# Kernel optimization log

Measured on AMD Instinct MI355X. Metric: run time of the kernel, lower is better.

Reference implementation:

```python
import jax, jax.numpy as jnp
import numpy as np
from jax import lax

B, H, W, C = 8, 128, 128, 256


def setup_inputs() -> dict:
    key = jax.random.key(0)
    k1, k2 = jax.random.split(key)
    x = jax.random.normal(k1, (B, H, W, C), dtype=jnp.float32)
    # small-magnitude kernel so predicted offsets stay moderate (like trained init)
    kernel = jax.random.normal(k2, (3, 3, C, 2 * C), dtype=jnp.float32) * 0.01
    bias = jnp.zeros((2 * C,), dtype=jnp.float32)
    return {"x": x, "kernel": kernel, "bias": bias}


def _deform_sample(x, kernel, bias):
    b, h, w, c = x.shape
    # offset prediction conv: (b,h,w,c) -> (b,h,w,2c), SAME padding, stride 1
    offsets = lax.conv_general_dilated(
        x, kernel, window_strides=(1, 1), padding="SAME",
        dimension_numbers=("NHWC", "HWIO", "NHWC")) + bias
    # faithful reshape scaffolding from the original keras layer
    # (b,h,w,2c) -> (b,2c,h,w) -> (b*c, h, w, 2)
    offs = jnp.transpose(offsets, (0, 3, 1, 2)).reshape(b * c, h, w, 2)
    # (b,h,w,c) -> (b*c, h, w)
    xb = jnp.transpose(x, (0, 3, 1, 2)).reshape(b * c, h, w)

    n = h * w
    offs = offs.reshape(b * c, n, 2)
    grid = jnp.stack(jnp.meshgrid(jnp.arange(h), jnp.arange(w), indexing="ij"), axis=-1)
    grid = grid.reshape(n, 2).astype(x.dtype)  # (n,2) absolute (i,j)
    coords = offs + grid  # (b*c, n, 2)

    # original clips coord0 by w-1 and coord1 by h-1 (h==w assumed)
    c0 = jnp.clip(coords[..., 0], 0.0, jnp.float32(w - 1))
    c1 = jnp.clip(coords[..., 1], 0.0, jnp.float32(h - 1))
    coords = jnp.stack([c0, c1], axis=-1)

    lt = jnp.floor(coords).astype(jnp.int32)  # (b*c, n, 2)
    rb = jnp.ceil(coords).astype(jnp.int32)

    bidx = jnp.arange(b * c)[:, None]  # (b*c, 1) broadcast over n
    vals_lt = xb[bidx, lt[..., 0], lt[..., 1]]
    vals_rb = xb[bidx, rb[..., 0], rb[..., 1]]
    vals_lb = xb[bidx, lt[..., 0], rb[..., 1]]
    vals_rt = xb[bidx, rb[..., 0], lt[..., 1]]

    frac = coords - lt.astype(coords.dtype)  # (b*c, n, 2)
    vals_t = vals_lt + (vals_rt - vals_lt) * frac[..., 0]
    vals_b = vals_lb + (vals_rb - vals_lb) * frac[..., 0]
    mapped = vals_t + (vals_b - vals_t) * frac[..., 1]  # (b*c, n)

    # (b*c, h*w) -> (b, c, h, w) -> (b, h, w, c)
    return jnp.transpose(mapped.reshape(b, c, h, w), (0, 2, 3, 1))


def reference(x, kernel, bias):
    return _deform_sample(x, kernel, bias)
```

## Files before the change

kernel.cpp:

```cpp
#include <hip/hip_runtime.h>
#include <hip/hip_bf16.h>

#define BATCH 8
#define HH 128
#define WW 128
#define CC 256
#define OCC 512

typedef __bf16 bf16x8 __attribute__((ext_vector_type(8)));
typedef float f32x4 __attribute__((ext_vector_type(4)));

__global__ void prep_weights(const float* __restrict__ k, __bf16* __restrict__ wt) {
    int idx = blockIdx.x * 256 + threadIdx.x;
    int oc   = idx & 511;
    int rest = idx >> 9;
    int ic   = rest & 255;
    int tap  = rest >> 8;
    wt[(tap * OCC + oc) * CC + ic] = (__bf16)k[idx];
}

__global__ __launch_bounds__(256, 2)
void conv_offset_sample(const float* __restrict__ x, const __bf16* __restrict__ wt,
                        const float* __restrict__ bias, float* __restrict__ out) {
    const int bi  = blockIdx.x;
    const int ncb = bi & 3;
    const int cr  = (bi >> 2) & 127;
    const int b   = bi >> 9;
    const int oc0 = ncb * 128;

    const int tid  = threadIdx.x;
    const int lane = tid & 63;
    const int wid  = tid >> 6;
    const int wm   = wid >> 1;
    const int wn   = wid & 1;
    const int l15  = lane & 15;
    const int lg   = lane >> 4;

    const float* xb = x + (size_t)b * (HH * WW * CC);

    f32x4 acc[4][4] = {};

#pragma unroll 1
    for (int tap = 0; tap < 9; ++tap) {
        const int dy = tap / 3 - 1;
        const int dx = tap - (tap / 3) * 3 - 1;
        const int row = cr + dy;
        const bool rowok = (unsigned)row < (unsigned)HH;
        const float* xrow = xb + row * (WW * CC);
        const __bf16* wtap = wt + (size_t)tap * (OCC * CC);

        for (int icc = 0; icc < CC; icc += 32) {
            const int ic = icc + lg * 8;

            bf16x8 afrag[4];
#pragma unroll
            for (int mi = 0; mi < 4; ++mi) {
                const int col = wm * 64 + mi * 16 + l15 + dx;
                f32x4 v0 = {0.f, 0.f, 0.f, 0.f};
                f32x4 v1 = {0.f, 0.f, 0.f, 0.f};
                if (rowok && (unsigned)col < (unsigned)WW) {
                    const f32x4* p = (const f32x4*)(xrow + col * CC + ic);
                    v0 = p[0];
                    v1 = p[1];
                }
                bf16x8 a;
                a[0] = (__bf16)v0[0]; a[1] = (__bf16)v0[1];
                a[2] = (__bf16)v0[2]; a[3] = (__bf16)v0[3];
                a[4] = (__bf16)v1[0]; a[5] = (__bf16)v1[1];
                a[6] = (__bf16)v1[2]; a[7] = (__bf16)v1[3];
                afrag[mi] = a;
            }

            bf16x8 bfrag[4];
#pragma unroll
            for (int ni = 0; ni < 4; ++ni) {
                const int oc = oc0 + wn * 64 + ni * 16 + l15;
                bfrag[ni] = *(const bf16x8*)(wtap + oc * CC + ic);
            }

#pragma unroll
            for (int mi = 0; mi < 4; ++mi)
#pragma unroll
                for (int ni = 0; ni < 4; ++ni)
                    acc[mi][ni] = __builtin_amdgcn_mfma_f32_16x16x32_bf16(
                        afrag[mi], bfrag[ni], acc[mi][ni], 0, 0, 0);
        }
    }

    const int ibase = cr >> 1;
    const int jbase = (cr & 1) * 64;

#pragma unroll
    for (int ni = 0; ni < 4; ++ni) {
        const int oc = oc0 + wn * 64 + ni * 16 + l15;
        const float bv = bias[oc];
        const int p  = oc >> 1;
        const int i2 = ibase + ((oc & 1) << 6);
        const float* xp = x + (size_t)b * (HH * WW * CC) + p;
        float* op = out + (((size_t)b * HH + i2) * WW) * CC + p;

#pragma unroll
        for (int mi = 0; mi < 4; ++mi) {
#pragma unroll
            for (int s = 0; s < 2; ++s) {
                const int u  = wm * 32 + mi * 8 + lg * 2 + s;
                const int j2 = jbase + u;

                float c0 = acc[mi][ni][2 * s]     + bv + (float)i2;
                float c1 = acc[mi][ni][2 * s + 1] + bv + (float)j2;
                c0 = fminf(fmaxf(c0, 0.f), 127.f);
                c1 = fminf(fmaxf(c1, 0.f), 127.f);

                const int lt0 = (int)floorf(c0);
                const int rb0 = (int)ceilf(c0);
                const int lt1 = (int)floorf(c1);
                const int rb1 = (int)ceilf(c1);
                const float f0 = c0 - (float)lt0;
                const float f1 = c1 - (float)lt1;

                const float vlt = xp[(lt0 * WW + lt1) * CC];
                const float vrb = xp[(rb0 * WW + rb1) * CC];
                const float vlb = xp[(lt0 * WW + rb1) * CC];
                const float vrt = xp[(rb0 * WW + lt1) * CC];

                const float vt = vlt + (vrt - vlt) * f0;
                const float vb = vlb + (vrb - vlb) * f0;
                op[(size_t)j2 * CC] = vt + (vb - vt) * f1;
            }
        }
    }
}

extern "C" void kernel_launch(void* const* d_in, const int* in_sizes, int n_in,
                              void* d_out, int out_size, void* d_ws, size_t ws_size,
                              hipStream_t stream) {
    const float* x    = (const float*)d_in[0];
    const float* kern = (const float*)d_in[1];
    const float* bias = (const float*)d_in[2];
    float* out = (float*)d_out;
    __bf16* wt = (__bf16*)d_ws;

    prep_weights<<<4608, 256, 0, stream>>>(kern, wt);
    conv_offset_sample<<<4096, 256, 0, stream>>>(x, wt, bias, out);
}
```

Measured before the change: 1.811 ms.

## Add planar transposed copy of x for gather sampling and reorder weight columns

Adds a transpose kernel that writes x in channel-planar layout (b,c,h*w) into workspace, so the bilinear gathers within a channel plane touch nearby addresses instead of addresses strided by 256 floats. Weight prep now permutes output channels so each block's N-tile groups channels by offset parity, which changes the channel-to-lane mapping in the epilogue. The transpose costs an extra full read and write of x (about 128MB each way) and needs a large workspace; if the workspace is too small the code falls back to the old interleaved layout. Launch bounds drop the min-blocks hint.

New measurement: 1.949 ms. 1.08x slower.

```diff
diff --git a/kernel.cpp b/kernel.cpp
--- a/kernel.cpp
+++ b/kernel.cpp
@@ -11,22 +11,49 @@
 typedef float f32x4 __attribute__((ext_vector_type(4)));
 
 __global__ void prep_weights(const float* __restrict__ k, __bf16* __restrict__ wt) {
-    int idx = blockIdx.x * 256 + threadIdx.x;
-    int oc   = idx & 511;
-    int rest = idx >> 9;
-    int ic   = rest & 255;
-    int tap  = rest >> 8;
-    wt[(tap * OCC + oc) * CC + ic] = (__bf16)k[idx];
+    const int n   = blockIdx.x & 511;
+    const int tap = blockIdx.x >> 9;
+    const int ic  = threadIdx.x;
+    const int oc  = ((n & 255) << 1) | (n >> 8);
+    wt[((size_t)(tap * OCC + n)) * CC + ic] = (__bf16)k[((size_t)(tap * CC + ic)) * OCC + oc];
 }
 
-__global__ __launch_bounds__(256, 2)
-void conv_offset_sample(const float* __restrict__ x, const __bf16* __restrict__ wt,
+__global__ __launch_bounds__(256)
+void transpose_x(const float* __restrict__ x, float* __restrict__ xt) {
+    __shared__ float tile[64][65];
+    const int pt = blockIdx.x & 3;
+    const int mt = (blockIdx.x >> 2) & 255;
+    const int b  = blockIdx.x >> 10;
+    const int m0 = mt * 64;
+    const int p0 = pt * 64;
+    const int tl = threadIdx.x & 63;
+    const int tr = threadIdx.x >> 6;
+
+    const float* xb = x + (size_t)b * (HH * WW * CC);
+#pragma unroll
+    for (int rr = 0; rr < 16; ++rr) {
+        const int m = rr * 4 + tr;
+        tile[m][tl] = xb[(size_t)(m0 + m) * CC + p0 + tl];
+    }
+    __syncthreads();
+    float* xtb = xt + (size_t)b * (CC * HH * WW);
+#pragma unroll
+    for (int rr = 0; rr < 16; ++rr) {
+        const int p = rr * 4 + tr;
+        xtb[(size_t)(p0 + p) * (HH * WW) + m0 + tl] = tile[tl][p];
+    }
+}
+
+template <bool PLANAR>
+__global__ __launch_bounds__(256)
+void conv_offset_sample(const float* __restrict__ x, const float* __restrict__ xt,
+                        const __bf16* __restrict__ wt,
                         const float* __restrict__ bias, float* __restrict__ out) {
     const int bi  = blockIdx.x;
     const int ncb = bi & 3;
     const int cr  = (bi >> 2) & 127;
     const int b   = bi >> 9;
-    const int oc0 = ncb * 128;
+    const int n0  = ncb * 128;
 
     const int tid  = threadIdx.x;
     const int lane = tid & 63;
@@ -74,8 +101,8 @@
             bf16x8 bfrag[4];
 #pragma unroll
             for (int ni = 0; ni < 4; ++ni) {
-                const int oc = oc0 + wn * 64 + ni * 16 + l15;
-                bfrag[ni] = *(const bf16x8*)(wtap + oc * CC + ic);
+                const int n = n0 + wn * 64 + ni * 16 + l15;
+                bfrag[ni] = *(const bf16x8*)(wtap + (size_t)n * CC + ic);
             }
 
 #pragma unroll
@@ -92,11 +119,18 @@
 
 #pragma unroll
     for (int ni = 0; ni < 4; ++ni) {
-        const int oc = oc0 + wn * 64 + ni * 16 + l15;
-        const float bv = bias[oc];
-        const int p  = oc >> 1;
-        const int i2 = ibase + ((oc & 1) << 6);
-        const float* xp = x + (size_t)b * (HH * WW * CC) + p;
+        const int n   = n0 + wn * 64 + ni * 16 + l15;
+        const int p   = n & 255;
+        const int par = n >> 8;
+        const int i2  = ibase + (par << 6);
+        const float bv = bias[2 * p + par];
+
+        const float* plane;
+        if (PLANAR) {
+            plane = xt + (size_t)(b * CC + p) * (HH * WW);
+        } else {
+            plane = x + (size_t)b * (HH * WW * CC) + p;
+        }
         float* op = out + (((size_t)b * HH + i2) * WW) * CC + p;
 
 #pragma unroll
@@ -118,10 +152,18 @@
                 const float f0 = c0 - (float)lt0;
                 const float f1 = c1 - (float)lt1;
 
-                const float vlt = xp[(lt0 * WW + lt1) * CC];
-                const float vrb = xp[(rb0 * WW + rb1) * CC];
-                const float vlb = xp[(lt0 * WW + rb1) * CC];
-                const float vrt = xp[(rb0 * WW + lt1) * CC];
+                float vlt, vrb, vlb, vrt;
+                if (PLANAR) {
+                    vlt = plane[(lt0 << 7) + lt1];
+                    vrb = plane[(rb0 << 7) + rb1];
+                    vlb = plane[(lt0 << 7) + rb1];
+                    vrt = plane[(rb0 << 7) + lt1];
+                } else {
+                    vlt = plane[((lt0 << 7) + lt1) << 8];
+                    vrb = plane[((rb0 << 7) + rb1) << 8];
+                    vlb = plane[((lt0 << 7) + rb1) << 8];
+                    vrt = plane[((rb0 << 7) + lt1) << 8];
+                }
 
                 const float vt = vlt + (vrt - vlt) * f0;
                 const float vb = vlb + (vrb - vlb) * f0;
@@ -138,8 +180,18 @@
     const float* kern = (const float*)d_in[1];
     const float* bias = (const float*)d_in[2];
     float* out = (float*)d_out;
+
     __bf16* wt = (__bf16*)d_ws;
+    const size_t XT_OFF = 4u * 1024u * 1024u;
+    const size_t XT_BYTES = (size_t)BATCH * CC * HH * WW * 4;
+    float* xt = (float*)((char*)d_ws + XT_OFF);
+    const bool planar = (ws_size >= XT_OFF + XT_BYTES);
 
     prep_weights<<<4608, 256, 0, stream>>>(kern, wt);
-    conv_offset_sample<<<4096, 256, 0, stream>>>(x, wt, bias, out);
+    if (planar) {
+        transpose_x<<<8192, 256, 0, stream>>>(x, xt);
+        conv_offset_sample<true><<<4096, 256, 0, stream>>>(x, xt, wt, bias, out);
+    } else {
+        conv_offset_sample<false><<<4096, 256, 0, stream>>>(x, xt, wt, bias, out);
+    }
 }
```

## Stage bf16 input rows in LDS and gather from a channel-planar bf16 copy

Applied to the files above, without the earlier changes.

Adds a prep pass that converts x to bf16 twice: once in NHWC layout and once transposed into per-channel planes. The conv kernel now stages whole bf16 input rows into double-buffered LDS with async global-to-LDS loads and an XOR swizzle. Each staged row is reused across the three horizontal taps, and the wave tiling changes to 2x8. The bilinear gather now reads 2-byte values from contiguous per-channel planes, replacing strided fp32 loads, and the block order is remapped. This trades extra prep passes and workspace traffic for less global load traffic, no per-tap fp32-to-bf16 conversion, and better gather locality. Gathered values are now bf16 rather than fp32, which lowers output precision.

Measured after the change: 1.488 ms. 1.22x faster.

```diff
diff --git a/kernel.cpp b/kernel.cpp
--- a/kernel.cpp
+++ b/kernel.cpp
@@ -8,105 +8,159 @@
 #define OCC 512
 
 typedef __bf16 bf16x8 __attribute__((ext_vector_type(8)));
+typedef unsigned int u32x4 __attribute__((ext_vector_type(4)));
 typedef float f32x4 __attribute__((ext_vector_type(4)));
 
+#define WT_OFF   0
+#define ZROW_OFF 2359296
+#define XTB_OFF  2424832
+#define XBF_OFF  69533696
+
 __global__ void prep_weights(const float* __restrict__ k, __bf16* __restrict__ wt) {
-    int idx = blockIdx.x * 256 + threadIdx.x;
-    int oc   = idx & 511;
-    int rest = idx >> 9;
-    int ic   = rest & 255;
-    int tap  = rest >> 8;
-    wt[(tap * OCC + oc) * CC + ic] = (__bf16)k[idx];
+    const int n   = blockIdx.x & 511;
+    const int tap = blockIdx.x >> 9;
+    const int ic  = threadIdx.x;
+    const int oc  = ((n & 255) << 1) | (n >> 8);
+    wt[((size_t)(tap * OCC + n)) * CC + ic] = (__bf16)k[((size_t)(tap * CC + ic)) * OCC + oc];
+}
+
+__global__ void zero_fill(float* __restrict__ z) {
+    z[blockIdx.x * 256 + threadIdx.x] = 0.0f;
+}
+
+__global__ __launch_bounds__(256)
+void prep_x(const float* __restrict__ x, __bf16* __restrict__ xbf, __bf16* __restrict__ xtb) {
+    __shared__ float tile[64][65];
+    const int pt = blockIdx.x & 3;
+    const int mt = (blockIdx.x >> 2) & 255;
+    const int b  = blockIdx.x >> 10;
+    const int m0 = mt * 64, p0 = pt * 64;
+    const int tl = threadIdx.x & 63, tr = threadIdx.x >> 6;
+
+    const float* xb = x + (size_t)b * (HH * WW * CC);
+    __bf16* xbfb = xbf + (size_t)b * (HH * WW * CC);
+#pragma unroll
+    for (int rr = 0; rr < 16; ++rr) {
+        const int m = rr * 4 + tr;
+        const float v = xb[(size_t)(m0 + m) * CC + p0 + tl];
+        tile[m][tl] = v;
+        xbfb[(size_t)(m0 + m) * CC + p0 + tl] = (__bf16)v;
+    }
+    __syncthreads();
+    __bf16* xtbb = xtb + (size_t)b * (CC * HH * WW);
+#pragma unroll
+    for (int rr = 0; rr < 16; ++rr) {
+        const int p = rr * 4 + tr;
+        xtbb[(size_t)(p0 + p) * (HH * WW) + m0 + tl] = (__bf16)tile[tl][p];
+    }
+}
+
+__device__ __forceinline__ void gload16(const void* g, void* l) {
+    __builtin_amdgcn_global_load_lds(
+        (const __attribute__((address_space(1))) void*)g,
+        (__attribute__((address_space(3))) void*)l, 16, 0, 0);
+}
+
+__device__ __forceinline__ void stage_chunk(const __bf16* __restrict__ srcrow, int h,
+                                            __bf16* ldsbuf, int wid, int lane) {
+    const int sub = lane >> 4;
+    const int icb = (lane & 15) * 16;
+#pragma unroll
+    for (int t = 0; t < 8; ++t) {
+        const int col = (wid * 8 + t) * 4 + sub;
+        const int srcoff = col * 512 + h * 256 + (icb ^ ((col & 7) << 4));
+        gload16((const char*)srcrow + srcoff, (char*)ldsbuf + (wid * 8 + t) * 1024);
+    }
 }
 
 __global__ __launch_bounds__(256, 2)
-void conv_offset_sample(const float* __restrict__ x, const __bf16* __restrict__ wt,
+void conv_offset_sample(const __bf16* __restrict__ xbf, const __bf16* __restrict__ xtb,
+                        const __bf16* __restrict__ zrow, const __bf16* __restrict__ wt,
                         const float* __restrict__ bias, float* __restrict__ out) {
-    const int bi  = blockIdx.x;
-    const int ncb = bi & 3;
-    const int cr  = (bi >> 2) & 127;
-    const int b   = bi >> 9;
-    const int oc0 = ncb * 128;
+    __shared__ __bf16 lds_a[2][16384];
+
+    const int orig = blockIdx.x;
+    const int bi = (orig & 7) * 512 + (orig >> 3);
+    const int nc = bi & 3;
+    const int cr = (bi >> 2) & 127;
+    const int b  = bi >> 9;
 
     const int tid  = threadIdx.x;
     const int lane = tid & 63;
     const int wid  = tid >> 6;
-    const int wm   = wid >> 1;
-    const int wn   = wid & 1;
     const int l15  = lane & 15;
     const int lg   = lane >> 4;
 
-    const float* xb = x + (size_t)b * (HH * WW * CC);
-
-    f32x4 acc[4][4] = {};
-
+    f32x4 acc[2][8] = {};
+
+    {
+        const int rg = cr - 1;
+        const __bf16* srcrow = ((unsigned)rg < 128u) ? xbf + ((size_t)(b * 128 + rg) << 15) : zrow;
+        stage_chunk(srcrow, 0, lds_a[0], wid, lane);
+    }
+    __syncthreads();
+
+    int cur = 0;
 #pragma unroll 1
-    for (int tap = 0; tap < 9; ++tap) {
-        const int dy = tap / 3 - 1;
-        const int dx = tap - (tap / 3) * 3 - 1;
-        const int row = cr + dy;
-        const bool rowok = (unsigned)row < (unsigned)HH;
-        const float* xrow = xb + row * (WW * CC);
-        const __bf16* wtap = wt + (size_t)tap * (OCC * CC);
-
-        for (int icc = 0; icc < CC; icc += 32) {
-            const int ic = icc + lg * 8;
-
-            bf16x8 afrag[4];
-#pragma unroll
-            for (int mi = 0; mi < 4; ++mi) {
-                const int col = wm * 64 + mi * 16 + l15 + dx;
-                f32x4 v0 = {0.f, 0.f, 0.f, 0.f};
-                f32x4 v1 = {0.f, 0.f, 0.f, 0.f};
-                if (rowok && (unsigned)col < (unsigned)WW) {
-                    const f32x4* p = (const f32x4*)(xrow + col * CC + ic);
-                    v0 = p[0];
-                    v1 = p[1];
+    for (int idx = 0; idx < 6; ++idx) {
+        if (idx < 5) {
+            const int n2 = idx + 1;
+            const int rg = cr + (n2 >> 1) - 1;
+            const __bf16* srcrow = ((unsigned)rg < 128u) ? xbf + ((size_t)(b * 128 + rg) << 15) : zrow;
+            stage_chunk(srcrow, n2 & 1, lds_a[cur ^ 1], wid, lane);
+        }
+        const int r = idx >> 1;
+        const int h = idx & 1;
+        const __bf16* Ab = lds_a[cur];
+        const int colb = wid * 32;
+
+#pragma unroll
+        for (int dx = 0; dx < 3; ++dx) {
+            const __bf16* wtap = wt + ((size_t)((r * 3 + dx) * OCC + nc * 128)) * CC + h * 128;
+#pragma unroll
+            for (int kk = 0; kk < 4; ++kk) {
+                bf16x8 a[2];
+#pragma unroll
+                for (int mi = 0; mi < 2; ++mi) {
+                    const int ca = colb + mi * 16 + l15 + dx - 1;
+                    const unsigned msk = ((unsigned)ca < 128u) ? 0xFFFFFFFFu : 0u;
+                    const int ad = (((ca & 127) << 8) + ((kk * 32 + lg * 8) << 1)) ^ ((ca & 7) << 4);
+                    u32x4 uv = *(const u32x4*)((const char*)Ab + ad);
+                    uv &= msk;
+                    a[mi] = __builtin_bit_cast(bf16x8, uv);
                 }
-                bf16x8 a;
-                a[0] = (__bf16)v0[0]; a[1] = (__bf16)v0[1];
-                a[2] = (__bf16)v0[2]; a[3] = (__bf16)v0[3];
-                a[4] = (__bf16)v1[0]; a[5] = (__bf16)v1[1];
-                a[6] = (__bf16)v1[2]; a[7] = (__bf16)v1[3];
-                afrag[mi] = a;
+#pragma unroll
+                for (int ni = 0; ni < 8; ++ni) {
+                    const bf16x8 bv = *(const bf16x8*)(wtap + (ni * 16 + l15) * CC + kk * 32 + lg * 8);
+                    acc[0][ni] = __builtin_amdgcn_mfma_f32_16x16x32_bf16(a[0], bv, acc[0][ni], 0, 0, 0);
+                    acc[1][ni] = __builtin_amdgcn_mfma_f32_16x16x32_bf16(a[1], bv, acc[1][ni], 0, 0, 0);
+                }
             }
-
-            bf16x8 bfrag[4];
-#pragma unroll
-            for (int ni = 0; ni < 4; ++ni) {
-                const int oc = oc0 + wn * 64 + ni * 16 + l15;
-                bfrag[ni] = *(const bf16x8*)(wtap + oc * CC + ic);
-            }
-
-#pragma unroll
-            for (int mi = 0; mi < 4; ++mi)
-#pragma unroll
-                for (int ni = 0; ni < 4; ++ni)
-                    acc[mi][ni] = __builtin_amdgcn_mfma_f32_16x16x32_bf16(
-                        afrag[mi], bfrag[ni], acc[mi][ni], 0, 0, 0);
         }
-    }
-
-    const int ibase = cr >> 1;
-    const int jbase = (cr & 1) * 64;
-
-#pragma unroll
-    for (int ni = 0; ni < 4; ++ni) {
-        const int oc = oc0 + wn * 64 + ni * 16 + l15;
-        const float bv = bias[oc];
-        const int p  = oc >> 1;
-        const int i2 = ibase + ((oc & 1) << 6);
-        const float* xp = x + (size_t)b * (HH * WW * CC) + p;
-        float* op = out + (((size_t)b * HH + i2) * WW) * CC + p;
-
-#pragma unroll
-        for (int mi = 0; mi < 4; ++mi) {
+        __syncthreads();
+        cur ^= 1;
+    }
+
+    const int jbase = (cr & 1) << 6;
+    const int par = nc >> 1;
+    const int i2  = (cr >> 1) + (par << 6);
+    const float fi2 = (float)i2;
+
+#pragma unroll
+    for (int ni = 0; ni < 8; ++ni) {
+        const int p = ((nc & 1) << 7) + ni * 16 + l15;
+        const float bv = bias[2 * p + par];
+        const __bf16* plane = xtb + ((size_t)(b * 256 + p) << 14);
+        float* op = out + (((size_t)(b * 128 + i2)) << 7) * 256 + p;
+
+#pragma unroll
+        for (int mi = 0; mi < 2; ++mi) {
 #pragma unroll
             for (int s = 0; s < 2; ++s) {
-                const int u  = wm * 32 + mi * 8 + lg * 2 + s;
+                const int u  = wid * 16 + mi * 8 + lg * 2 + s;
                 const int j2 = jbase + u;
 
-                float c0 = acc[mi][ni][2 * s]     + bv + (float)i2;
+                float c0 = acc[mi][ni][2 * s]     + bv + fi2;
                 float c1 = acc[mi][ni][2 * s + 1] + bv + (float)j2;
                 c0 = fminf(fmaxf(c0, 0.f), 127.f);
                 c1 = fminf(fmaxf(c1, 0.f), 127.f);
@@ -118,14 +172,14 @@
                 const float f0 = c0 - (float)lt0;
                 const float f1 = c1 - (float)lt1;
 
-                const float vlt = xp[(lt0 * WW + lt1) * CC];
-                const float vrb = xp[(rb0 * WW + rb1) * CC];
-                const float vlb = xp[(lt0 * WW + rb1) * CC];
-                const float vrt = xp[(rb0 * WW + lt1) * CC];
+                const float vlt = (float)plane[(lt0 << 7) + lt1];
+                const float vrb = (float)plane[(rb0 << 7) + rb1];
+                const float vlb = (float)plane[(lt0 << 7) + rb1];
+                const float vrt = (float)plane[(rb0 << 7) + lt1];
 
                 const float vt = vlt + (vrt - vlt) * f0;
                 const float vb = vlb + (vrb - vlb) * f0;
-                op[(size_t)j2 * CC] = vt + (vb - vt) * f1;
+                op[(size_t)j2 * 256] = vt + (vb - vt) * f1;
             }
         }
     }
@@ -138,8 +192,14 @@
     const float* kern = (const float*)d_in[1];
     const float* bias = (const float*)d_in[2];
     float* out = (float*)d_out;
-    __bf16* wt = (__bf16*)d_ws;
+
+    __bf16* wt   = (__bf16*)((char*)d_ws + WT_OFF);
+    __bf16* zrow = (__bf16*)((char*)d_ws + ZROW_OFF);
+    __bf16* xtb  = (__bf16*)((char*)d_ws + XTB_OFF);
+    __bf16* xbf  = (__bf16*)((char*)d_ws + XBF_OFF);
 
     prep_weights<<<4608, 256, 0, stream>>>(kern, wt);
-    conv_offset_sample<<<4096, 256, 0, stream>>>(x, wt, bias, out);
-}
+    zero_fill<<<64, 256, 0, stream>>>((float*)zrow);
+    prep_x<<<8192, 256, 0, stream>>>(x, xbf, xtb);
+    conv_offset_sample<<<4096, 256, 0, stream>>>(xbf, xtb, zrow, wt, bias, out);
+}
```
